# Performance work log

Hardware: AMD Instinct MI355X
Metric: run time of the kernel (lower is better)

The kernel has to match this reference:

```python
import jax, jax.numpy as jnp
import numpy as np

D_MODEL = 1024
N_HEADS = 16
D_K = D_MODEL // N_HEADS  # 64
SCALE = 1.0 / np.sqrt(D_K).astype(np.float32)


def setup_inputs() -> dict:
    key = jax.random.key(0)
    kx, kq, kk, kv, ko = jax.random.split(key, 5)
    B, S = 2, 2048
    s = 0.02  # keep pre-softmax logits in a sane range
    return {
        "x": jax.random.normal(kx, (B, S, D_MODEL), dtype=jnp.float32),
        "Wq": jax.random.normal(kq, (D_MODEL, D_MODEL), dtype=jnp.float32) * s,
        "Wk": jax.random.normal(kk, (D_MODEL, D_MODEL), dtype=jnp.float32) * s,
        "Wv": jax.random.normal(kv, (D_MODEL, D_MODEL), dtype=jnp.float32) * s,
        "Wo": jax.random.normal(ko, (D_MODEL, D_MODEL), dtype=jnp.float32) * s,
    }


def reference(x, Wq, Wk, Wv, Wo):
    # x: [B, S, D]; nn.Linear(bias=False) computes x @ W.T
    B, S, D = x.shape
    H, dk = N_HEADS, D_K

    def proj(W):
        # [B, S, D] -> [B, H, S, dk]
        return (x @ W.T).reshape(B, S, H, dk).transpose(0, 2, 1, 3)

    q = proj(Wq)
    k = proj(Wk)
    v = proj(Wv)

    # Flash tiling with online softmax is exact full attention (no mask):
    scores = jnp.einsum("bhqd,bhkd->bhqk", q, k) * SCALE  # [B,H,S,S]
    p = jax.nn.softmax(scores, axis=-1)
    o = jnp.einsum("bhqk,bhkd->bhqd", p, v)               # [B,H,S,dk]

    o = o.transpose(0, 2, 1, 3).reshape(B, S, D)
    return o @ Wo.T
```

## Files before the change

kernel.cpp:

```cpp
#include <hip/hip_runtime.h>
#include <cstdint>
#include <type_traits>

typedef __attribute__((ext_vector_type(8))) __bf16 bf16x8;
typedef __attribute__((ext_vector_type(4))) float f32x4;
typedef __attribute__((ext_vector_type(4))) short s16x4;
using u16 = unsigned short;
using u32 = unsigned int;

#define D_MODEL 1024
#define N_HEADS 16
#define D_K     64
#define SEQ     2048
#define BATCH   2
#define NTOKENS (BATCH * SEQ)
#define SCALE   0.125f
#define LOG2E   1.44269504088896340736f
#define C2      (SCALE * LOG2E)

__device__ __forceinline__ u16 f32_to_bf16(float f) {
    union { float f; u32 u; } v; v.f = f;
    u32 r = (v.u + 0x7fffu + ((v.u >> 16) & 1u)) >> 16;
    return (u16)r;
}

__device__ __forceinline__ u32 pack_bf16_pair(float a, float b) {
    u32 ua = __builtin_bit_cast(u32, a) + 0x8000u;
    u32 ub = __builtin_bit_cast(u32, b) + 0x8000u;
    return __builtin_amdgcn_perm(ub, ua, 0x07060302);
}

typedef const __attribute__((address_space(1))) u32* gas_ptr;
typedef __attribute__((address_space(3))) u32* las_ptr;
__device__ __forceinline__ void gl2lds16(const u16* g, u16* l) {
    __builtin_amdgcn_global_load_lds((gas_ptr)g, (las_ptr)l, 16, 0, 0);
}

__global__ __launch_bounds__(256) void cvt_all(const float* __restrict__ x,
                                               const float* __restrict__ Wq, const float* __restrict__ Wk,
                                               const float* __restrict__ Wv, const float* __restrict__ Wo,
                                               u16* __restrict__ xb,
                                               u16* __restrict__ wq, u16* __restrict__ wk,
                                               u16* __restrict__ wv, u16* __restrict__ wo) {
    const int NX = NTOKENS * D_MODEL;
    size_t i = (size_t)(blockIdx.x * 256 + threadIdx.x) * 4;
    const float* src; u16* dst; size_t off;
    if (i < (size_t)NX) { src = x; dst = xb; off = i; }
    else {
        size_t j = i - NX;
        int w = (int)(j >> 20);
        off = j & ((1u << 20) - 1);
        src = (w == 0) ? Wq : (w == 1) ? Wk : (w == 2) ? Wv : Wo;
        dst = (w == 0) ? wq : (w == 1) ? wk : (w == 2) ? wv : wo;
    }
    float4 f = *(const float4*)(src + off);
    u32 lo = (u32)f32_to_bf16(f.x) | ((u32)f32_to_bf16(f.y) << 16);
    u32 hi = (u32)f32_to_bf16(f.z) | ((u32)f32_to_bf16(f.w) << 16);
    uint2 o; o.x = lo; o.y = hi;
    *(uint2*)(dst + off) = o;
}

__global__ __launch_bounds__(256) void gemm_qkv(const u16* __restrict__ xb,
                                                const u16* __restrict__ wq,
                                                const u16* __restrict__ wk,
                                                const u16* __restrict__ wv,
                                                u16* __restrict__ Qb, u16* __restrict__ Kb,
                                                u16* __restrict__ Vt) {
    __shared__ __align__(16) u16 As[128 * 32];
    __shared__ __align__(16) u16 Bs[128 * 32];

    const int tid  = threadIdx.x;
    const int wave = tid >> 6, lane = tid & 63;
    const int quad = lane >> 4, l4 = lane & 15;
    const int wm = wave >> 1, wn = wave & 1;
    const int f = blockIdx.x;

    const u16 *Abase, *Bbase;
    if (f < 512) {
        const int m0 = (f & 31) * 128, t = f >> 5;
        Abase = xb + (size_t)m0 * D_MODEL;
        Bbase = ((t < 8) ? wq : wk) + (size_t)(t & 7) * 128 * D_MODEL;
    } else {
        const int g = f - 512;
        Abase = wv + (size_t)(g & 7) * 128 * D_MODEL;
        Bbase = xb + (size_t)(g >> 3) * 128 * D_MODEL;
    }

    f32x4 acc[4][4] = {};

    const int r0 = wave * 16 + (lane >> 2);
    const int ch = (lane & 3) * 8;
    const u16* Ag0 = Abase + (size_t)r0 * D_MODEL + ch;
    const u16* Bg0 = Bbase + (size_t)r0 * D_MODEL + ch;
    u16* AsW = As + wave * 512;
    u16* BsW = Bs + wave * 512;

    for (int kt = 0; kt < 32; ++kt) {
        const int ko = kt * 32;
        __syncthreads();
        gl2lds16(Ag0 + ko, AsW);
        gl2lds16(Ag0 + (size_t)64 * D_MODEL + ko, AsW + 2048);
        gl2lds16(Bg0 + ko, BsW);
        gl2lds16(Bg0 + (size_t)64 * D_MODEL + ko, BsW + 2048);
        __syncthreads();

        bf16x8 af[4], bfr[4];
#pragma unroll
        for (int mt = 0; mt < 4; mt++)
            af[mt] = *(const bf16x8*)&As[(wm * 64 + mt * 16 + l4) * 32 + quad * 8];
#pragma unroll
        for (int nt = 0; nt < 4; nt++)
            bfr[nt] = *(const bf16x8*)&Bs[(wn * 64 + nt * 16 + l4) * 32 + quad * 8];
#pragma unroll
        for (int mt = 0; mt < 4; mt++)
#pragma unroll
            for (int nt = 0; nt < 4; nt++)
                acc[mt][nt] = __builtin_amdgcn_mfma_f32_16x16x32_bf16(af[mt], bfr[nt], acc[mt][nt], 0, 0, 0);
    }

#pragma unroll
    for (int mt = 0; mt < 4; mt++)
#pragma unroll
        for (int nt = 0; nt < 4; nt++)
#pragma unroll
            for (int r = 0; r < 4; r++) {
                int mrow = wm * 64 + mt * 16 + quad * 4 + r;
                int ncol = wn * 64 + nt * 16 + l4;
                float v = acc[mt][nt][r];
                if (f < 512) {
                    const int m0 = (f & 31) * 128, t = f >> 5;
                    if (t < 8)
                        Qb[(size_t)(m0 + mrow) * D_MODEL + (t & 7) * 128 + ncol] = f32_to_bf16(v * C2);
                    else
                        Kb[(size_t)(m0 + mrow) * D_MODEL + (t & 7) * 128 + ncol] = f32_to_bf16(v);
                } else {
                    const int g = f - 512;
                    Vt[(size_t)((g & 7) * 128 + mrow) * NTOKENS + (g >> 3) * 128 + ncol] = f32_to_bf16(v);
                }
            }
}

__global__ __launch_bounds__(256) void gemm_out(const u16* __restrict__ A,
                                                const u16* __restrict__ Bw,
                                                float* __restrict__ C) {
    __shared__ __align__(16) u16 As[64 * 32];
    __shared__ __align__(16) u16 Bs[128 * 32];

    const int tid  = threadIdx.x;
    const int wave = tid >> 6, lane = tid & 63;
    const int quad = lane >> 4, l4 = lane & 15;
    const int m0 = blockIdx.y * 64, n0 = blockIdx.x * 128;

    f32x4 acc[4][2] = {};

    const int r0 = wave * 16 + (lane >> 2);
    const int ch = (lane & 3) * 8;
    const u16* Ag0 = A  + (size_t)(m0 + r0) * D_MODEL + ch;
    const u16* Bg0 = Bw + (size_t)(n0 + r0) * D_MODEL + ch;
    u16* AsW = As + wave * 512;
    u16* BsW = Bs + wave * 512;

    for (int kt = 0; kt < 32; ++kt) {
        const int ko = kt * 32;
        __syncthreads();
        gl2lds16(Ag0 + ko, AsW);
        gl2lds16(Bg0 + ko, BsW);
        gl2lds16(Bg0 + (size_t)64 * D_MODEL + ko, BsW + 2048);
        __syncthreads();

        bf16x8 af[4], bfr[2];
#pragma unroll
        for (int mt = 0; mt < 4; mt++)
            af[mt] = *(const bf16x8*)&As[(mt * 16 + l4) * 32 + quad * 8];
#pragma unroll
        for (int nt = 0; nt < 2; nt++)
            bfr[nt] = *(const bf16x8*)&Bs[(wave * 32 + nt * 16 + l4) * 32 + quad * 8];
#pragma unroll
        for (int mt = 0; mt < 4; mt++)
#pragma unroll
            for (int nt = 0; nt < 2; nt++)
                acc[mt][nt] = __builtin_amdgcn_mfma_f32_16x16x32_bf16(af[mt], bfr[nt], acc[mt][nt], 0, 0, 0);
    }

#pragma unroll
    for (int mt = 0; mt < 4; mt++)
#pragma unroll
        for (int nt = 0; nt < 2; nt++)
#pragma unroll
            for (int r = 0; r < 4; r++) {
                int m = m0 + mt * 16 + quad * 4 + r;
                int n = n0 + wave * 32 + nt * 16 + l4;
                C[(size_t)m * D_MODEL + n] = acc[mt][nt][r];
            }
}

__global__ __launch_bounds__(512, 4) void attn(const u16* __restrict__ Q,
                                               const u16* __restrict__ K,
                                               const u16* __restrict__ Vt,
                                               u16* __restrict__ O) {
    __shared__ __align__(16) u16 smem[4 * 64 * 72];
    u16* KsB = smem;
    u16* VsB = smem + 2 * 64 * 72;

    const int tid  = threadIdx.x;
    const int wave = tid >> 6, lane = tid & 63;
    const int quad = lane >> 4, l4 = lane & 15;
    const int qg = wave & 3, kv = wave >> 2;
    const int bid = blockIdx.x;
    const int h  = (bid & 7) | (((bid >> 3) & 1) << 3);
    const int b  = (bid >> 4) & 1;
    const int q0 = (bid >> 5) * 128;
    const size_t headoff = (size_t)b * SEQ * D_MODEL + (size_t)h * D_K;

    const int sarr = tid >> 8;
    const int st   = tid & 255;
    const int srow = st >> 2, schk = (st & 3) * 16;
    const u16* gsrc = (sarr == 0)
        ? K  + headoff + (size_t)srow * D_MODEL + schk
        : Vt + (size_t)(h * 64 + srow) * NTOKENS + (size_t)b * SEQ + schk;
    const size_t gstep = (sarr == 0) ? (size_t)64 * D_MODEL : 64;
    u16* lds0 = ((sarr == 0) ? KsB : VsB) + srow * 72 + schk;
    u16* lds1 = lds0 + 64 * 72;

    bf16x8 qa[2][2];
#pragma unroll
    for (int qs = 0; qs < 2; qs++) {
        const u16* qp = Q + headoff + (size_t)(q0 + qg * 32 + qs * 16 + l4) * D_MODEL + quad * 8;
        qa[qs][0] = *(const bf16x8*)qp;
        qa[qs][1] = *(const bf16x8*)(qp + 32);
    }

    int4 pr0 = *(const int4*)gsrc;
    int4 pr1 = *(const int4*)(gsrc + 8);

    f32x4 acc_o[2][4] = {};
    float lsum[2] = {0.f, 0.f};

    for (int it = 0; it < 32; ++it) {
        u16* dst = (it & 1) ? lds1 : lds0;
        *(int4*)dst       = pr0;
        *(int4*)(dst + 8) = pr1;
        __syncthreads();

        const u16* gn = gsrc + (size_t)((it + 1) & 31) * gstep;
        pr0 = *(const int4*)gn;
        pr1 = *(const int4*)(gn + 8);

        const u16* ksr = KsB + (it & 1) * (64 * 72);
        const u16* vsr = VsB + (it & 1) * (64 * 72);

        f32x4 sacc[2][2] = {};
#pragma unroll
        for (int n2 = 0; n2 < 2; n2++) {
            const int krow = kv * 32 + n2 * 16 + l4;
            bf16x8 kb0 = *(const bf16x8*)&ksr[krow * 72 + quad * 8];
            bf16x8 kb1 = *(const bf16x8*)&ksr[krow * 72 + 32 + quad * 8];
#pragma unroll
            for (int qs = 0; qs < 2; qs++) {
                sacc[qs][n2] = __builtin_amdgcn_mfma_f32_16x16x32_bf16(kb0, qa[qs][0], sacc[qs][n2], 0, 0, 0);
                sacc[qs][n2] = __builtin_amdgcn_mfma_f32_16x16x32_bf16(kb1, qa[qs][1], sacc[qs][n2], 0, 0, 0);
            }
        }

        s16x4 pf[2][2];
#pragma unroll
        for (int qs = 0; qs < 2; qs++)
#pragma unroll
            for (int n2 = 0; n2 < 2; n2++) {
                float p0 = __builtin_amdgcn_exp2f(sacc[qs][n2][0]);
                float p1 = __builtin_amdgcn_exp2f(sacc[qs][n2][1]);
                float p2 = __builtin_amdgcn_exp2f(sacc[qs][n2][2]);
                float p3 = __builtin_amdgcn_exp2f(sacc[qs][n2][3]);
                lsum[qs] += (p0 + p1) + (p2 + p3);
                union { u32 u[2]; s16x4 v; } pp;
                pp.u[0] = pack_bf16_pair(p0, p1);
                pp.u[1] = pack_bf16_pair(p2, p3);
                pf[qs][n2] = pp.v;
            }

#pragma unroll
        for (int n2 = 0; n2 < 2; n2++)
#pragma unroll
            for (int dvt = 0; dvt < 4; dvt++) {
                s16x4 vfr = *(const s16x4*)&vsr[(dvt * 16 + l4) * 72 + kv * 32 + n2 * 16 + quad * 4];
#pragma unroll
                for (int qs = 0; qs < 2; qs++)
                    acc_o[qs][dvt] = __builtin_amdgcn_mfma_f32_16x16x16bf16_1k(pf[qs][n2], vfr, acc_o[qs][dvt], 0, 0, 0);
            }
    }

#pragma unroll
    for (int qs = 0; qs < 2; qs++) {
        lsum[qs] += __shfl_xor(lsum[qs], 16, 64);
        lsum[qs] += __shfl_xor(lsum[qs], 32, 64);
    }

    float* Of = (float*)smem;
    float* Lf = (float*)(smem + 16384);
    __syncthreads();
    if (kv == 1) {
#pragma unroll
        for (int qs = 0; qs < 2; qs++) {
#pragma unroll
            for (int dvt = 0; dvt < 4; dvt++)
#pragma unroll
                for (int r = 0; r < 4; r++)
                    Of[(qg * 32 + qs * 16 + quad * 4 + r) * 64 + dvt * 16 + l4] = acc_o[qs][dvt][r];
            if (quad == 0) Lf[qg * 32 + qs * 16 + l4] = lsum[qs];
        }
    }
    __syncthreads();
    if (kv == 0) {
#pragma unroll
        for (int qs = 0; qs < 2; qs++) {
            float ltot = lsum[qs] + Lf[qg * 32 + qs * 16 + l4];
#pragma unroll
            for (int r = 0; r < 4; r++) {
                float linv = 1.f / __shfl(ltot, quad * 4 + r, 64);
                int qrow = q0 + qg * 32 + qs * 16 + quad * 4 + r;
#pragma unroll
                for (int dvt = 0; dvt < 4; dvt++) {
                    float v = acc_o[qs][dvt][r] +
                              Of[(qg * 32 + qs * 16 + quad * 4 + r) * 64 + dvt * 16 + l4];
                    O[headoff + (size_t)qrow * D_MODEL + dvt * 16 + l4] = f32_to_bf16(v * linv);
                }
            }
        }
    }
}

extern "C" void kernel_launch(void* const* d_in, const int* in_sizes, int n_in,
                              void* d_out, int out_size, void* d_ws, size_t ws_size,
                              hipStream_t stream) {
    const float* x  = (const float*)d_in[0];
    const float* Wq = (const float*)d_in[1];
    const float* Wk = (const float*)d_in[2];
    const float* Wv = (const float*)d_in[3];
    const float* Wo = (const float*)d_in[4];

    const int NW = D_MODEL * D_MODEL;

    char* ws = (char*)d_ws;
    u16* xb = (u16*)ws;
    u16* wq = (u16*)(ws + (8u << 20));
    u16* wk = wq + NW;
    u16* wv = wk + NW;
    u16* wo = wv + NW;
    u16* Qb  = (u16*)(ws + (16u << 20));
    u16* Kb  = (u16*)(ws + (24u << 20));
    u16* Vtb = (u16*)(ws + (32u << 20));

    cvt_all<<<8192, 256, 0, stream>>>(x, Wq, Wk, Wv, Wo, xb, wq, wk, wv, wo);

    gemm_qkv<<<768, 256, 0, stream>>>(xb, wq, wk, wv, Qb, Kb, Vtb);

    attn<<<512, 512, 0, stream>>>(Qb, Kb, Vtb, xb);

    gemm_out<<<dim3(8, 64), 256, 0, stream>>>(xb, wo, (float*)d_out);
}
```

Measured before the change: 202.3 us.

## Use K=32 MFMA for PV, compute row sums via ones-row MFMA, widen QKV k-step

The attention kernel now lays out V in LDS so each lane reads 8 contiguous keys, letting P·V use the 16x16x32 MFMA instead of two 16x16x16 ones. The softmax denominator is computed on the matrix units by multiplying P against an extra LDS row of ones, which removes the scalar row-sum adds and the cross-lane shuffles. The QKV GEMM loads two 32-wide K slices per barrier pair, halving the barrier count at the cost of more LDS. The ones-row trick adds LDS space and extra MFMAs, and V stores into LDS are now split into 8-byte writes.

```diff
diff --git a/kernel.cpp b/kernel.cpp
--- a/kernel.cpp
+++ b/kernel.cpp
@@ -4,7 +4,6 @@
 
 typedef __attribute__((ext_vector_type(8))) __bf16 bf16x8;
 typedef __attribute__((ext_vector_type(4))) float f32x4;
-typedef __attribute__((ext_vector_type(4))) short s16x4;
 using u16 = unsigned short;
 using u32 = unsigned int;
 
@@ -66,8 +65,8 @@
                                                 const u16* __restrict__ wv,
                                                 u16* __restrict__ Qb, u16* __restrict__ Kb,
                                                 u16* __restrict__ Vt) {
-    __shared__ __align__(16) u16 As[128 * 32];
-    __shared__ __align__(16) u16 Bs[128 * 32];
+    __shared__ __align__(16) u16 As[2][128 * 32];
+    __shared__ __align__(16) u16 Bs[2][128 * 32];
 
     const int tid  = threadIdx.x;
     const int wave = tid >> 6, lane = tid & 63;
@@ -92,30 +91,39 @@
     const int ch = (lane & 3) * 8;
     const u16* Ag0 = Abase + (size_t)r0 * D_MODEL + ch;
     const u16* Bg0 = Bbase + (size_t)r0 * D_MODEL + ch;
-    u16* AsW = As + wave * 512;
-    u16* BsW = Bs + wave * 512;
-
-    for (int kt = 0; kt < 32; ++kt) {
-        const int ko = kt * 32;
-        __syncthreads();
-        gl2lds16(Ag0 + ko, AsW);
-        gl2lds16(Ag0 + (size_t)64 * D_MODEL + ko, AsW + 2048);
-        gl2lds16(Bg0 + ko, BsW);
-        gl2lds16(Bg0 + (size_t)64 * D_MODEL + ko, BsW + 2048);
-        __syncthreads();
-
-        bf16x8 af[4], bfr[4];
-#pragma unroll
-        for (int mt = 0; mt < 4; mt++)
-            af[mt] = *(const bf16x8*)&As[(wm * 64 + mt * 16 + l4) * 32 + quad * 8];
-#pragma unroll
-        for (int nt = 0; nt < 4; nt++)
-            bfr[nt] = *(const bf16x8*)&Bs[(wn * 64 + nt * 16 + l4) * 32 + quad * 8];
-#pragma unroll
-        for (int mt = 0; mt < 4; mt++)
+    u16* AsW0 = As[0] + wave * 512;
+    u16* AsW1 = As[1] + wave * 512;
+    u16* BsW0 = Bs[0] + wave * 512;
+    u16* BsW1 = Bs[1] + wave * 512;
+
+    for (int kt = 0; kt < 16; ++kt) {
+        const int ko = kt * 64;
+        __syncthreads();
+        gl2lds16(Ag0 + ko, AsW0);
+        gl2lds16(Ag0 + (size_t)64 * D_MODEL + ko, AsW0 + 2048);
+        gl2lds16(Bg0 + ko, BsW0);
+        gl2lds16(Bg0 + (size_t)64 * D_MODEL + ko, BsW0 + 2048);
+        gl2lds16(Ag0 + ko + 32, AsW1);
+        gl2lds16(Ag0 + (size_t)64 * D_MODEL + ko + 32, AsW1 + 2048);
+        gl2lds16(Bg0 + ko + 32, BsW1);
+        gl2lds16(Bg0 + (size_t)64 * D_MODEL + ko + 32, BsW1 + 2048);
+        __syncthreads();
+
+#pragma unroll
+        for (int s = 0; s < 2; ++s) {
+            bf16x8 af[4], bfr[4];
+#pragma unroll
+            for (int mt = 0; mt < 4; mt++)
+                af[mt] = *(const bf16x8*)&As[s][(wm * 64 + mt * 16 + l4) * 32 + quad * 8];
 #pragma unroll
             for (int nt = 0; nt < 4; nt++)
-                acc[mt][nt] = __builtin_amdgcn_mfma_f32_16x16x32_bf16(af[mt], bfr[nt], acc[mt][nt], 0, 0, 0);
+                bfr[nt] = *(const bf16x8*)&Bs[s][(wn * 64 + nt * 16 + l4) * 32 + quad * 8];
+#pragma unroll
+            for (int mt = 0; mt < 4; mt++)
+#pragma unroll
+                for (int nt = 0; nt < 4; nt++)
+                    acc[mt][nt] = __builtin_amdgcn_mfma_f32_16x16x32_bf16(af[mt], bfr[nt], acc[mt][nt], 0, 0, 0);
+        }
     }
 
 #pragma unroll
@@ -198,9 +206,10 @@
                                                const u16* __restrict__ K,
                                                const u16* __restrict__ Vt,
                                                u16* __restrict__ O) {
-    __shared__ __align__(16) u16 smem[4 * 64 * 72];
+    __shared__ __align__(16) u16 smem[2 * 64 * 72 + 2 * 80 * 72];
     u16* KsB = smem;
     u16* VsB = smem + 2 * 64 * 72;
+    const int KBUF = 64 * 72, VBUF = 80 * 72;
 
     const int tid  = threadIdx.x;
     const int wave = tid >> 6, lane = tid & 63;
@@ -212,15 +221,20 @@
     const int q0 = (bid >> 5) * 128;
     const size_t headoff = (size_t)b * SEQ * D_MODEL + (size_t)h * D_K;
 
+    for (int i = tid; i < 2 * 16 * 72; i += 512) {
+        int buf = i / (16 * 72), rem = i % (16 * 72);
+        VsB[buf * VBUF + (64 + rem / 72) * 72 + (rem % 72)] = (rem / 72 == 0) ? (u16)0x3F80 : (u16)0;
+    }
+
     const int sarr = tid >> 8;
     const int st   = tid & 255;
-    const int srow = st >> 2, schk = (st & 3) * 16;
+    const int srow = st >> 2, sc = st & 3;
     const u16* gsrc = (sarr == 0)
-        ? K  + headoff + (size_t)srow * D_MODEL + schk
-        : Vt + (size_t)(h * 64 + srow) * NTOKENS + (size_t)b * SEQ + schk;
+        ? K  + headoff + (size_t)srow * D_MODEL + sc * 16
+        : Vt + (size_t)(h * 64 + srow) * NTOKENS + (size_t)b * SEQ + sc * 16;
     const size_t gstep = (sarr == 0) ? (size_t)64 * D_MODEL : 64;
-    u16* lds0 = ((sarr == 0) ? KsB : VsB) + srow * 72 + schk;
-    u16* lds1 = lds0 + 64 * 72;
+    u16* kw0 = KsB + srow * 72 + sc * 16;
+    u16* vw0 = VsB + srow * 72 + (sc >> 1) * 32 + (sc & 1) * 4;
 
     bf16x8 qa[2][2];
 #pragma unroll
@@ -234,20 +248,30 @@
     int4 pr1 = *(const int4*)(gsrc + 8);
 
     f32x4 acc_o[2][4] = {};
-    float lsum[2] = {0.f, 0.f};
+    f32x4 acc_l[2] = {};
 
     for (int it = 0; it < 32; ++it) {
-        u16* dst = (it & 1) ? lds1 : lds0;
-        *(int4*)dst       = pr0;
-        *(int4*)(dst + 8) = pr1;
+        if (sarr == 0) {
+            u16* d = kw0 + (it & 1) * KBUF;
+            *(int4*)d       = pr0;
+            *(int4*)(d + 8) = pr1;
+        } else {
+            u16* d = vw0 + (it & 1) * VBUF;
+            const uint2* h0 = (const uint2*)&pr0;
+            const uint2* h1 = (const uint2*)&pr1;
+            *(uint2*)(d)      = h0[0];
+            *(uint2*)(d + 8)  = h0[1];
+            *(uint2*)(d + 16) = h1[0];
+            *(uint2*)(d + 24) = h1[1];
+        }
         __syncthreads();
 
         const u16* gn = gsrc + (size_t)((it + 1) & 31) * gstep;
         pr0 = *(const int4*)gn;
         pr1 = *(const int4*)(gn + 8);
 
-        const u16* ksr = KsB + (it & 1) * (64 * 72);
-        const u16* vsr = VsB + (it & 1) * (64 * 72);
+        const u16* ksr = KsB + (it & 1) * KBUF;
+        const u16* vsr = VsB + (it & 1) * VBUF;
 
         f32x4 sacc[2][2] = {};
 #pragma unroll
@@ -262,7 +286,7 @@
             }
         }
 
-        s16x4 pf[2][2];
+        union { u32 u[4]; bf16x8 v; } pp[2];
 #pragma unroll
         for (int qs = 0; qs < 2; qs++)
 #pragma unroll
@@ -271,28 +295,23 @@
                 float p1 = __builtin_amdgcn_exp2f(sacc[qs][n2][1]);
                 float p2 = __builtin_amdgcn_exp2f(sacc[qs][n2][2]);
                 float p3 = __builtin_amdgcn_exp2f(sacc[qs][n2][3]);
-                lsum[qs] += (p0 + p1) + (p2 + p3);
-                union { u32 u[2]; s16x4 v; } pp;
-                pp.u[0] = pack_bf16_pair(p0, p1);
-                pp.u[1] = pack_bf16_pair(p2, p3);
-                pf[qs][n2] = pp.v;
-            }
-
-#pragma unroll
-        for (int n2 = 0; n2 < 2; n2++)
-#pragma unroll
-            for (int dvt = 0; dvt < 4; dvt++) {
-                s16x4 vfr = *(const s16x4*)&vsr[(dvt * 16 + l4) * 72 + kv * 32 + n2 * 16 + quad * 4];
-#pragma unroll
-                for (int qs = 0; qs < 2; qs++)
-                    acc_o[qs][dvt] = __builtin_amdgcn_mfma_f32_16x16x16bf16_1k(pf[qs][n2], vfr, acc_o[qs][dvt], 0, 0, 0);
-            }
-    }
-
-#pragma unroll
-    for (int qs = 0; qs < 2; qs++) {
-        lsum[qs] += __shfl_xor(lsum[qs], 16, 64);
-        lsum[qs] += __shfl_xor(lsum[qs], 32, 64);
+                pp[qs].u[n2 * 2]     = pack_bf16_pair(p0, p1);
+                pp[qs].u[n2 * 2 + 1] = pack_bf16_pair(p2, p3);
+            }
+
+#pragma unroll
+        for (int dvt = 0; dvt < 4; dvt++) {
+            bf16x8 vfr = *(const bf16x8*)&vsr[(dvt * 16 + l4) * 72 + kv * 32 + quad * 8];
+#pragma unroll
+            for (int qs = 0; qs < 2; qs++)
+                acc_o[qs][dvt] = __builtin_amdgcn_mfma_f32_16x16x32_bf16(pp[qs].v, vfr, acc_o[qs][dvt], 0, 0, 0);
+        }
+        {
+            bf16x8 ofr = *(const bf16x8*)&vsr[(64 + l4) * 72 + kv * 32 + quad * 8];
+#pragma unroll
+            for (int qs = 0; qs < 2; qs++)
+                acc_l[qs] = __builtin_amdgcn_mfma_f32_16x16x32_bf16(pp[qs].v, ofr, acc_l[qs], 0, 0, 0);
+        }
     }
 
     float* Of = (float*)smem;
@@ -306,17 +325,21 @@
 #pragma unroll
                 for (int r = 0; r < 4; r++)
                     Of[(qg * 32 + qs * 16 + quad * 4 + r) * 64 + dvt * 16 + l4] = acc_o[qs][dvt][r];
-            if (quad == 0) Lf[qg * 32 + qs * 16 + l4] = lsum[qs];
+            if (l4 == 0)
+#pragma unroll
+                for (int r = 0; r < 4; r++)
+                    Lf[qg * 32 + qs * 16 + quad * 4 + r] = acc_l[qs][r];
         }
     }
     __syncthreads();
     if (kv == 0) {
 #pragma unroll
-        for (int qs = 0; qs < 2; qs++) {
-            float ltot = lsum[qs] + Lf[qg * 32 + qs * 16 + l4];
+        for (int qs = 0; qs < 2; qs++)
 #pragma unroll
             for (int r = 0; r < 4; r++) {
-                float linv = 1.f / __shfl(ltot, quad * 4 + r, 64);
+                float lown = __shfl(acc_l[qs][r], quad * 16, 64);
+                float ltot = lown + Lf[qg * 32 + qs * 16 + quad * 4 + r];
+                float linv = 1.f / ltot;
                 int qrow = q0 + qg * 32 + qs * 16 + quad * 4 + r;
 #pragma unroll
                 for (int dvt = 0; dvt < 4; dvt++) {
@@ -325,7 +348,6 @@
                     O[headoff + (size_t)qrow * D_MODEL + dvt * 16 + l4] = f32_to_bf16(v * linv);
                 }
             }
-        }
     }
 }
 
```

Measured after the change: 189.1 us. 1.07x faster.
